# Optimization experiments

Measured on AMD Instinct MI355X. Metric: run time of the kernel, lower is better.

Reference implementation:

```python
import jax, jax.numpy as jnp
import numpy as np

DIM = 1536
NHEADS = 24
HEAD_DIM = DIM // NHEADS
EPS = 1e-6


def rms_norm(x):
    # normalize over last dim, no learned weight
    ms = jnp.mean(x * x, axis=-1, keepdims=True)
    return x * jax.lax.rsqrt(ms + EPS)


def rope_non_neox(x, cos, sin):
    # x: [B, S, H, D]; cos/sin: [S, D] -> broadcast [1, S, 1, D]
    # non-neox (GPT-J / interleaved) style: pairs are (x0,x1),(x2,x3),...
    c = cos[None, :, None, :]
    s = sin[None, :, None, :]
    x1 = x[..., 0::2]
    x2 = x[..., 1::2]
    c1 = c[..., 0::2]
    s1 = s[..., 0::2]
    o1 = x1 * c1 - x2 * s1
    o2 = x2 * c1 + x1 * s1
    out = jnp.stack([o1, o2], axis=-1).reshape(x.shape)
    return out


def setup_inputs() -> dict:
    key = jax.random.key(0)
    k1, k2, k3, k4, k5 = jax.random.split(key, 5)
    B, S = 4, 4096
    x = jax.random.normal(k1, (B, S, DIM), dtype=jnp.float32)
    # rotary tables: build valid cos/sin from random angles (interleaved duplication)
    half = HEAD_DIM // 2
    inv_freq = 1.0 / (10000.0 ** (jnp.arange(0, half, dtype=jnp.float32) / half))
    t = jnp.arange(S, dtype=jnp.float32)
    freqs = jnp.outer(t, inv_freq)  # [S, D/2]
    cos = jnp.repeat(jnp.cos(freqs), 2, axis=-1)  # [S, D] interleaved
    sin = jnp.repeat(jnp.sin(freqs), 2, axis=-1)
    w_qkv = jax.random.normal(k2, (DIM, 3 * DIM), dtype=jnp.float32) * (DIM ** -0.5)
    b_qkv = jax.random.normal(k3, (3 * DIM,), dtype=jnp.float32) * 0.02
    return {"x": x, "cos": cos, "sin": sin, "w_qkv": w_qkv, "b_qkv": b_qkv}


def reference(x, cos, sin, w_qkv, b_qkv):
    B, S, _ = x.shape
    H, D = NHEADS, HEAD_DIM
    qkv = jnp.einsum('bsd,de->bse', x, w_qkv) + b_qkv  # [B,S,3*DIM]
    q, k, v = jnp.split(qkv, 3, axis=-1)
    q = q.reshape(B, S, H, D)
    k = k.reshape(B, S, H, D)
    v = v.reshape(B, S, H, D)
    q = rms_norm(q)
    k = rms_norm(k)
    q = rope_non_neox(q, cos, sin)
    k = rope_non_neox(k, cos, sin)
    # SDPA: [B,H,S,D]
    qh = q.transpose(0, 2, 1, 3)
    kh = k.transpose(0, 2, 1, 3)
    vh = v.transpose(0, 2, 1, 3)
    scale = D ** -0.5
    scores = jnp.einsum('bhqd,bhkd->bhqk', qh, kh) * scale
    attn = jax.nn.softmax(scores, axis=-1)
    out = jnp.einsum('bhqk,bhkd->bhqd', attn, vh)
    out = out.transpose(0, 2, 1, 3).reshape(B, S, H * D)
    return out
```

## Files before the change

kernel.cpp:

```cpp
#include <hip/hip_runtime.h>

#define DIM   1536
#define NQKV  4608
#define NH    24
#define HD    64
#define BATCH 4
#define SEQ   4096
#define ROWS  16384

typedef _Float16 f16x8 __attribute__((ext_vector_type(8)));
typedef _Float16 f16x2 __attribute__((ext_vector_type(2)));
typedef __fp16   h16x2 __attribute__((ext_vector_type(2)));
typedef float    f32x4 __attribute__((ext_vector_type(4)));
typedef float    f32x16 __attribute__((ext_vector_type(16)));
typedef unsigned u32x2 __attribute__((ext_vector_type(2)));

__device__ __forceinline__ void gload_lds16(const void* g, void* l) {
  __builtin_amdgcn_global_load_lds(
      (const __attribute__((address_space(1))) unsigned int*)g,
      (__attribute__((address_space(3))) unsigned int*)l, 16, 0, 0);
}
__device__ __forceinline__ float fexp2(float x) {
#if __has_builtin(__builtin_amdgcn_exp2f)
  return __builtin_amdgcn_exp2f(x);
#else
  return exp2f(x);
#endif
}

__device__ __forceinline__ void swap32(unsigned& a, unsigned& b) {
#if __has_builtin(__builtin_amdgcn_permlane32_swap)
  u32x2 r = __builtin_amdgcn_permlane32_swap(a, b, false, false);
  a = r[0]; b = r[1];
#else
  const int hi = (threadIdx.x & 63) >> 5;
  unsigned as = (unsigned)__shfl_xor((int)a, 32);
  unsigned bs = (unsigned)__shfl_xor((int)b, 32);
  unsigned na = hi ? bs : a;
  unsigned nb = hi ? b  : as;
  a = na; b = nb;
#endif
}

#define QSCALE 0.18033688011112042f

__global__ __launch_bounds__(256) void convert_x(const float* __restrict__ X,
                                                 _Float16* __restrict__ Xh) {
  const int i = (blockIdx.x * 256 + threadIdx.x) * 8;
  float4 a = *(const float4*)(X + i);
  float4 b = *(const float4*)(X + i + 4);
  f16x8 h;
  h[0] = (_Float16)a.x; h[1] = (_Float16)a.y; h[2] = (_Float16)a.z; h[3] = (_Float16)a.w;
  h[4] = (_Float16)b.x; h[5] = (_Float16)b.y; h[6] = (_Float16)b.z; h[7] = (_Float16)b.w;
  *(f16x8*)(Xh + i) = h;
}

__global__ __launch_bounds__(256) void transpose_w(const float* __restrict__ W,
                                                   _Float16* __restrict__ Wt) {
  __shared__ float tile[32][33];
  const int tx = threadIdx.x, ty = threadIdx.y;
  const int k0 = blockIdx.y * 32, n0 = blockIdx.x * 32;
  #pragma unroll
  for (int i = 0; i < 32; i += 8)
    tile[ty + i][tx] = W[(size_t)(k0 + ty + i) * NQKV + n0 + tx];
  __syncthreads();
  #pragma unroll
  for (int i = 0; i < 32; i += 8)
    Wt[(size_t)(n0 + ty + i) * DIM + k0 + tx] = (_Float16)tile[tx][ty + i];
}

__global__ __launch_bounds__(256) void qkv_gemm(const _Float16* __restrict__ Xh,
                                                const _Float16* __restrict__ Wt,
                                                const float* __restrict__ Bias,
                                                const float* __restrict__ Cos,
                                                const float* __restrict__ Sin,
                                                _Float16* __restrict__ QKV) {
  __shared__ _Float16 As[128 * 64];
  __shared__ _Float16 Bs[128 * 64];
  const int w    = threadIdx.x >> 6;
  const int lane = threadIdx.x & 63;
  const int lr   = lane >> 3, lc = lane & 7;
  const int quad = lane >> 4, l15 = lane & 15;
  const int m0 = blockIdx.y * 128;
  const int n0 = blockIdx.x * 128;
  const int waveR = (w >> 1) * 64;
  const int waveC = (w & 1) * 64;

  f32x4 acc[4][4];
  #pragma unroll
  for (int i = 0; i < 4; i++)
    #pragma unroll
    for (int j = 0; j < 4; j++) acc[i][j] = (f32x4){0.f, 0.f, 0.f, 0.f};

  for (int kt = 0; kt < DIM / 64; ++kt) {
    const int k0 = kt * 64;
    #pragma unroll
    for (int i = 0; i < 4; ++i) {
      const int rr = w * 32 + i * 8;
      gload_lds16(Xh + (size_t)(m0 + rr + lr) * DIM + k0 + lc * 8, &As[rr * 64]);
      gload_lds16(Wt + (size_t)(n0 + rr + lr) * DIM + k0 + lc * 8, &Bs[rr * 64]);
    }
    __syncthreads();
    #pragma unroll
    for (int ks = 0; ks < 2; ++ks) {
      f16x8 aF[4], bF[4];
      #pragma unroll
      for (int t = 0; t < 4; t++)
        aF[t] = *(const f16x8*)&As[(waveR + t * 16 + l15) * 64 + ks * 32 + quad * 8];
      #pragma unroll
      for (int t = 0; t < 4; t++)
        bF[t] = *(const f16x8*)&Bs[(waveC + t * 16 + l15) * 64 + ks * 32 + quad * 8];
      #pragma unroll
      for (int mt = 0; mt < 4; mt++)
        #pragma unroll
        for (int nt = 0; nt < 4; nt++)
          acc[mt][nt] = __builtin_amdgcn_mfma_f32_16x16x32_f16(aF[mt], bF[nt], acc[mt][nt], 0, 0, 0);
    }
    __syncthreads();
  }

  const int nCol0  = n0 + waveC;
  const int region = nCol0 / DIM;

  float bias[4];
  #pragma unroll
  for (int nt = 0; nt < 4; nt++) bias[nt] = Bias[nCol0 + nt * 16 + l15];

  if (region == 2) {
    #pragma unroll
    for (int nt = 0; nt < 4; nt++) {
      const int n = nCol0 + nt * 16 + l15;
      #pragma unroll
      for (int mt = 0; mt < 4; mt++) {
        const int mBase = m0 + waveR + mt * 16 + quad * 4;
        #pragma unroll
        for (int r = 0; r < 4; r++)
          QKV[(size_t)(mBase + r) * NQKV + n] = (_Float16)(acc[mt][nt][r] + bias[nt]);
      }
    }
  } else {
    const float qsc = (region == 0) ? QSCALE : 1.0f;
    #pragma unroll
    for (int mt = 0; mt < 4; mt++) {
      const int mBase = m0 + waveR + mt * 16 + quad * 4;
      #pragma unroll
      for (int r = 0; r < 4; r++) {
        const int m = mBase + r;
        const int s = m & (SEQ - 1);
        float v[4];
        float ss = 0.f;
        #pragma unroll
        for (int nt = 0; nt < 4; nt++) {
          v[nt] = acc[mt][nt][r] + bias[nt];
          ss += v[nt] * v[nt];
        }
        #pragma unroll
        for (int off = 1; off < 16; off <<= 1) ss += __shfl_xor(ss, off);
        const float rinv = rsqrtf(ss * (1.f / 64.f) + 1e-6f);
        #pragma unroll
        for (int nt = 0; nt < 4; nt++) {
          const int d = nt * 16 + l15;
          const float c  = Cos[s * HD + d];
          const float si = Sin[s * HD + d];
          const float x  = v[nt] * rinv;
          const float xp = __shfl_xor(x, 1);
          float o = (l15 & 1) ? (x * c + xp * si) : (x * c - xp * si);
          o *= qsc;
          QKV[(size_t)m * NQKV + nCol0 + d] = (_Float16)o;
        }
      }
    }
  }
}

#define LSTR 72
__global__ __launch_bounds__(256) void flash_attn(const _Float16* __restrict__ QKV,
                                                  float* __restrict__ Out) {
  __shared__ __align__(16) _Float16 sm[2 * 64 * LSTR];
  _Float16* Ks  = sm;
  _Float16* Vts = sm + 64 * LSTR;
  const int w    = threadIdx.x >> 6;
  const int lane = threadIdx.x & 63;
  const int l31  = lane & 31;
  const int hi   = lane >> 5;
  const int qt = blockIdx.x;
  const int bh = blockIdx.y;
  const int b  = bh / NH;
  const int h  = bh - b * NH;
  const size_t rowb = (size_t)b * SEQ * NQKV + (size_t)h * HD;

  f16x8 qreg[4];
  {
    const int row = qt * 128 + w * 32 + l31;
    #pragma unroll
    for (int dw = 0; dw < 4; dw++)
      qreg[dw] = *(const f16x8*)(QKV + rowb + (size_t)row * NQKV + dw * 16 + hi * 8);
  }

  f32x16 o[2] = {};
  float ls0 = 0.f, ls1 = 0.f;
  const f16x2 one2 = {(_Float16)1.0f, (_Float16)1.0f};

  for (int kt = 0; kt < SEQ / 64; ++kt) {
    __syncthreads();
    #pragma unroll
    for (int i = 0; i < 2; i++) {
      const int chunk = threadIdx.x + i * 256;
      const int r = chunk >> 3, c0 = (chunk & 7) * 8;
      *(uint4*)&Ks[r * LSTR + c0] =
          *(const uint4*)(QKV + rowb + (size_t)(kt * 64 + r) * NQKV + DIM + c0);
    }
    #pragma unroll
    for (int i = 0; i < 2; i++) {
      const int c0 = w * 16 + i * 8;
      union { uint4 v; _Float16 u[8]; } d;
      d.v = *(const uint4*)(QKV + rowb + (size_t)(kt * 64 + lane) * NQKV + 2 * DIM + c0);
      #pragma unroll
      for (int j = 0; j < 8; j++) Vts[(c0 + j) * LSTR + lane] = d.u[j];
    }
    __syncthreads();

    #pragma unroll
    for (int kt32 = 0; kt32 < 2; ++kt32) {
      f32x16 sacc = {};
      #pragma unroll
      for (int dw = 0; dw < 4; dw++) {
        f16x8 kF = *(const f16x8*)&Ks[(kt32 * 32 + l31) * LSTR + dw * 16 + hi * 8];
        sacc = __builtin_amdgcn_mfma_f32_32x32x16_f16(kF, qreg[dw], sacc, 0, 0, 0);
      }

      unsigned pk[8];
      #pragma unroll
      for (int i = 0; i < 8; i++) {
        union { h16x2 h2; f16x2 f2; unsigned u; } uu;
#if __has_builtin(__builtin_amdgcn_cvt_pkrtz)
        uu.h2 = __builtin_amdgcn_cvt_pkrtz(fexp2(sacc[2 * i]), fexp2(sacc[2 * i + 1]));
#else
        uu.f2[0] = (_Float16)fexp2(sacc[2 * i]);
        uu.f2[1] = (_Float16)fexp2(sacc[2 * i + 1]);
#endif
        pk[i] = uu.u;
#if __has_builtin(__builtin_amdgcn_fdot2)
        if (i & 1) ls1 = __builtin_amdgcn_fdot2(uu.f2, one2, ls1, false);
        else       ls0 = __builtin_amdgcn_fdot2(uu.f2, one2, ls0, false);
#else
        if (i & 1) ls1 += (float)uu.f2[0] + (float)uu.f2[1];
        else       ls0 += (float)uu.f2[0] + (float)uu.f2[1];
#endif
      }
      swap32(pk[0], pk[2]);
      swap32(pk[1], pk[3]);
      swap32(pk[4], pk[6]);
      swap32(pk[5], pk[7]);

      #pragma unroll
      for (int h16 = 0; h16 < 2; ++h16) {
        const int kw = kt32 * 2 + h16;
        union { unsigned u[4]; f16x8 f; } pa;
        pa.u[0] = pk[h16 * 4 + 0];
        pa.u[1] = pk[h16 * 4 + 1];
        pa.u[2] = pk[h16 * 4 + 2];
        pa.u[3] = pk[h16 * 4 + 3];
        #pragma unroll
        for (int dt = 0; dt < 2; ++dt) {
          f16x8 vF = *(const f16x8*)&Vts[(dt * 32 + l31) * LSTR + kw * 16 + hi * 8];
          o[dt] = __builtin_amdgcn_mfma_f32_32x32x16_f16(pa.f, vF, o[dt], 0, 0, 0);
        }
      }
    }
  }

  const float lsum = ls0 + ls1;
  const float ls = lsum + __shfl_xor(lsum, 32);
  #pragma unroll
  for (int r = 0; r < 16; r++) {
    const int q = (r & 3) + 8 * (r >> 2) + 4 * hi;
    const float lrow = __shfl(ls, q);
    const int srow = qt * 128 + w * 32 + q;
    #pragma unroll
    for (int dt = 0; dt < 2; dt++)
      Out[((size_t)(b * SEQ + srow)) * DIM + h * HD + dt * 32 + l31] = o[dt][r] / lrow;
  }
}

extern "C" void kernel_launch(void* const* d_in, const int* in_sizes, int n_in,
                              void* d_out, int out_size, void* d_ws, size_t ws_size,
                              hipStream_t stream) {
  const float* X    = (const float*)d_in[0];
  const float* Cos  = (const float*)d_in[1];
  const float* Sin  = (const float*)d_in[2];
  const float* W    = (const float*)d_in[3];
  const float* Bias = (const float*)d_in[4];
  float* Out = (float*)d_out;

  char* ws = (char*)d_ws;
  _Float16* Xh  = (_Float16*)(ws);
  _Float16* Wt  = (_Float16*)(ws + 50331648);
  _Float16* QKV = (_Float16*)(ws + 64487424);

  convert_x  <<<dim3(ROWS * DIM / (8 * 256)), 256, 0, stream>>>(X, Xh);
  transpose_w<<<dim3(NQKV / 32, DIM / 32), dim3(32, 8), 0, stream>>>(W, Wt);
  qkv_gemm   <<<dim3(NQKV / 128, ROWS / 128), 256, 0, stream>>>(Xh, Wt, Bias, Cos, Sin, QKV);
  flash_attn <<<dim3(SEQ / 128, BATCH * NH), 256, 0, stream>>>(QKV, Out);
}
```

Before: 1.056 ms.

## Double-buffer K/V tiles in flash attention with register prefetch

The flash attention loop now prefetches the next K and V tile from global memory into registers before computing on the current tile. After the compute it writes them into the alternate LDS buffer, so one barrier per iteration replaces two. This is meant to hide global load latency behind the MFMA and softmax work. LDS usage doubles and register pressure rises, which may lower occupancy.

```diff
diff --git a/kernel.cpp b/kernel.cpp
--- a/kernel.cpp
+++ b/kernel.cpp
@@ -174,13 +174,14 @@
 }
 
 #define LSTR 72
+#define NT   (SEQ / 64)
+#define BUFH (2 * 64 * LSTR)
 __global__ __launch_bounds__(256) void flash_attn(const _Float16* __restrict__ QKV,
                                                   float* __restrict__ Out) {
-  __shared__ __align__(16) _Float16 sm[2 * 64 * LSTR];
-  _Float16* Ks  = sm;
-  _Float16* Vts = sm + 64 * LSTR;
-  const int w    = threadIdx.x >> 6;
-  const int lane = threadIdx.x & 63;
+  __shared__ __align__(16) _Float16 sm[2 * BUFH];
+  const int tid  = threadIdx.x;
+  const int w    = tid >> 6;
+  const int lane = tid & 63;
   const int l31  = lane & 31;
   const int hi   = lane >> 5;
   const int qt = blockIdx.x;
@@ -197,28 +198,53 @@
       qreg[dw] = *(const f16x8*)(QKV + rowb + (size_t)row * NQKV + dw * 16 + hi * 8);
   }
 
+  const _Float16* kp0 = QKV + rowb + (size_t)(tid >> 3) * NQKV + DIM + (tid & 7) * 8;
+  const _Float16* kp1 = kp0 + (size_t)32 * NQKV;
+  const _Float16* vp  = QKV + rowb + (size_t)lane * NQKV + 2 * DIM + w * 16;
+  const int kofs = (tid >> 3) * LSTR + (tid & 7) * 8;
+  const int vofs = (w * 16) * LSTR + lane;
+
+  uint4 kpre0, kpre1, vpre0, vpre1;
+  #define LOADREGS() do {                          \
+    kpre0 = *(const uint4*)kp0;                    \
+    kpre1 = *(const uint4*)kp1;                    \
+    vpre0 = *(const uint4*)vp;                     \
+    vpre1 = *(const uint4*)(vp + 8);               \
+  } while (0)
+  #define WRITEREGS(bufbase) do {                                   \
+    _Float16* Kb = (bufbase);                                       \
+    *(uint4*)&Kb[kofs] = kpre0;                                     \
+    *(uint4*)&Kb[kofs + 32 * LSTR] = kpre1;                         \
+    _Float16* Vb = (bufbase) + 64 * LSTR;                           \
+    union { uint4 v; _Float16 u[8]; } d0, d1;                       \
+    d0.v = vpre0; d1.v = vpre1;                                     \
+    _Pragma("unroll")                                               \
+    for (int j = 0; j < 8; j++) {                                   \
+      Vb[vofs + j * LSTR] = d0.u[j];                                \
+      Vb[vofs + (8 + j) * LSTR] = d1.u[j];                          \
+    }                                                               \
+  } while (0)
+
   f32x16 o[2] = {};
   float ls0 = 0.f, ls1 = 0.f;
   const f16x2 one2 = {(_Float16)1.0f, (_Float16)1.0f};
 
-  for (int kt = 0; kt < SEQ / 64; ++kt) {
-    __syncthreads();
-    #pragma unroll
-    for (int i = 0; i < 2; i++) {
-      const int chunk = threadIdx.x + i * 256;
-      const int r = chunk >> 3, c0 = (chunk & 7) * 8;
-      *(uint4*)&Ks[r * LSTR + c0] =
-          *(const uint4*)(QKV + rowb + (size_t)(kt * 64 + r) * NQKV + DIM + c0);
-    }
-    #pragma unroll
-    for (int i = 0; i < 2; i++) {
-      const int c0 = w * 16 + i * 8;
-      union { uint4 v; _Float16 u[8]; } d;
-      d.v = *(const uint4*)(QKV + rowb + (size_t)(kt * 64 + lane) * NQKV + 2 * DIM + c0);
-      #pragma unroll
-      for (int j = 0; j < 8; j++) Vts[(c0 + j) * LSTR + lane] = d.u[j];
-    }
-    __syncthreads();
+  LOADREGS();
+  WRITEREGS(sm);
+  __syncthreads();
+
+  int cur = 0;
+  for (int kt = 0; kt < NT; ++kt) {
+    const bool more = (kt + 1 < NT);
+    if (more) {
+      kp0 += (size_t)64 * NQKV;
+      kp1 += (size_t)64 * NQKV;
+      vp  += (size_t)64 * NQKV;
+      LOADREGS();
+    }
+
+    const _Float16* Ks  = sm + cur * BUFH;
+    const _Float16* Vts = Ks + 64 * LSTR;
 
     #pragma unroll
     for (int kt32 = 0; kt32 < 2; ++kt32) {
@@ -268,6 +294,10 @@
         }
       }
     }
+
+    if (more) WRITEREGS(sm + (cur ^ 1) * BUFH);
+    __syncthreads();
+    cur ^= 1;
   }
 
   const float lsum = ls0 + ls1;
@@ -281,6 +311,8 @@
     for (int dt = 0; dt < 2; dt++)
       Out[((size_t)(b * SEQ + srow)) * DIM + h * HD + dt * 32 + l31] = o[dt][r] / lrow;
   }
+  #undef LOADREGS
+  #undef WRITEREGS
 }
 
 extern "C" void kernel_launch(void* const* d_in, const int* in_sizes, int n_in,
```

After: 1.076 ms. Within noise of the previous version (+1.9%).
